# Kernel tuning notes

Measured on AMD Instinct MI355X. Metric: run time of the kernel, lower is better.

Reference implementation:

```python
import jax, jax.numpy as jnp
import numpy as np


def setup_inputs() -> dict:
    key = jax.random.key(0)
    k1, k2, k3 = jax.random.split(key, 3)
    C_in, C_out, K = 64, 64, 3
    x = jax.random.normal(k1, (32, C_in, 128, 128), dtype=jnp.float32)
    # Conv2d default init scale: U(-b, b) with b = 1/sqrt(fan_in)
    bound = 1.0 / np.sqrt(C_in * K * K)
    conv_weight = jax.random.uniform(k2, (C_out, C_in, K, K), dtype=jnp.float32,
                                     minval=-bound, maxval=bound)
    conv_bias = jax.random.uniform(k3, (C_out,), dtype=jnp.float32,
                                   minval=-bound, maxval=bound)
    return {"x": x, "conv_weight": conv_weight, "conv_bias": conv_bias}


def reference(x, conv_weight, conv_bias):
    # Conv2d, stride=1, padding=0 (VALID), NCHW/OIHW
    y = jax.lax.conv_general_dilated(
        x, conv_weight,
        window_strides=(1, 1), padding="VALID",
        dimension_numbers=("NCHW", "OIHW", "NCHW"),
    ) + conv_bias[None, :, None, None]
    # min over output channels (keepdim) then double tanh
    m = jnp.min(y, axis=1, keepdims=True)  # (N, 1, OH, OW)
    return jnp.tanh(jnp.tanh(m))
```

## Files before the change

kernel.cpp:

```cpp
#include <hip/hip_runtime.h>
#include <hip/hip_bf16.h>
#include <math.h>

typedef __attribute__((ext_vector_type(8))) short     short8;
typedef __attribute__((ext_vector_type(8))) __bf16    bf16x8;
typedef __attribute__((ext_vector_type(4))) float     f32x4;
typedef __attribute__((ext_vector_type(2))) unsigned int u32x2;

#define NB 32
#define CI 64
#define CO 64
#define H  128
#define W  128
#define OH 126
#define OW 126
#define HW (H*W)

#define TROWS 6
#define TCOLS 66
#define LDS_BYTES (TROWS*TCOLS*CI*2)

__device__ __forceinline__ unsigned int f2bf(float f) {
    unsigned int u = __builtin_bit_cast(unsigned int, f);
    u += 0x7fffu + ((u >> 16) & 1u);
    return u >> 16;
}

__device__ __forceinline__ unsigned int cvt_pk_bf16(float lo, float hi) {
    unsigned int r;
    asm("v_cvt_pk_bf16_f32 %0, %1, %2" : "=v"(r) : "v"(lo), "v"(hi));
    return r;
}

__device__ __forceinline__ float fast_tanh(float x) {
    float e = __builtin_amdgcn_exp2f(x * 2.8853900817779268f);
    float r = __builtin_amdgcn_rcpf(e + 1.0f);
    return 1.0f - 2.0f * r;
}

__global__ void wxform(const float* __restrict__ w, unsigned short* __restrict__ ws) {
    int tid = blockIdx.x * 256 + threadIdx.x;
    if (tid >= 18*4*64*8) return;
    int j   = tid & 7;
    int l   = (tid >> 3) & 63;
    int cf  = (tid >> 9) & 3;
    int ks  = tid >> 11;
    int co  = cf*16 + (l & 15);
    int ci  = (ks & 1)*32 + ((l >> 4) << 3) + j;
    int khw = ks >> 1;
    int kh  = khw / 3, kw = khw % 3;
    float v = w[co*(CI*9) + ci*9 + kh*3 + kw];
    ws[tid] = (unsigned short)f2bf(v);
}

__global__ __launch_bounds__(256, 3)
void conv_min_tanh(const float* __restrict__ x,
                   const unsigned short* __restrict__ wfrag,
                   const float* __restrict__ bias,
                   float* __restrict__ out) {
    __shared__ __align__(16) char xs[LDS_BYTES];

    const int lane   = threadIdx.x & 63;
    const int wv     = threadIdx.x >> 6;
    const int c0     = blockIdx.x * 64;
    const int r0     = blockIdx.y * 4;
    const int b      = blockIdx.z;

    const float* xb = x + b*CI*HW;

    float v[24][4];
    #pragma unroll
    for (int i = 0; i < 24; ++i) {
        const int task = wv + 4*i;
        const int r    = task >> 4;
        const int ci0  = (task & 15) << 2;
        const int gr   = r0 + r;
        v[i][0] = 0.f; v[i][1] = 0.f; v[i][2] = 0.f; v[i][3] = 0.f;
        if (gr < H) {
            const float* xp = xb + ci0*HW + gr*W + c0 + lane;
            v[i][0] = xp[0]; v[i][1] = xp[HW]; v[i][2] = xp[2*HW]; v[i][3] = xp[3*HW];
        }
    }
    const int t = threadIdx.x;
    float h0=0.f, h1=0.f, h2=0.f, h3=0.f;
    int hpix = 0, hci0 = 0;
    const bool hdo = t < 192;
    if (hdo) {
        const int r   = t >> 5;
        const int sub = t & 31;
        const int gc  = c0 + 64 + (sub & 1);
        hci0 = (sub >> 1) << 2;
        const int gr  = r0 + r;
        hpix = r*TCOLS + 64 + (sub & 1);
        if (gr < H && gc < W) {
            const float* xq = xb + hci0*HW + gr*W + gc;
            h0 = xq[0]; h1 = xq[HW]; h2 = xq[2*HW]; h3 = xq[3*HW];
        }
    }

    #pragma unroll
    for (int i = 0; i < 24; ++i) {
        const int task = wv + 4*i;
        const int r    = task >> 4;
        const int ci0  = (task & 15) << 2;
        int pix  = r*TCOLS + lane;
        int addr = (pix << 7) + (ci0 << 1);
        addr ^= (pix & 7) << 4;
        u32x2 pk; pk.x = cvt_pk_bf16(v[i][0], v[i][1]); pk.y = cvt_pk_bf16(v[i][2], v[i][3]);
        *(u32x2*)(xs + addr) = pk;
    }
    if (hdo) {
        int addr = (hpix << 7) + (hci0 << 1);
        addr ^= (hpix & 7) << 4;
        u32x2 qk; qk.x = cvt_pk_bf16(h0, h1); qk.y = cvt_pk_bf16(h2, h3);
        *(u32x2*)(xs + addr) = qk;
    }

    const short8* wp = (const short8*)wfrag;
    short8 wf[2][2][4];
    #pragma unroll
    for (int k2 = 0; k2 < 2; ++k2)
        #pragma unroll
        for (int cf = 0; cf < 4; ++cf)
            wf[0][k2][cf] = wp[(k2*4 + cf)*64 + lane];

    __syncthreads();

    const int orow = r0 + wv;
    if (orow >= OH) return;

    const int lane_c = lane & 15;
    const int hi16   = (lane >> 4) << 4;

    int abase[9][2];
    #pragma unroll
    for (int kh = 0; kh < 3; ++kh)
        #pragma unroll
        for (int kw = 0; kw < 3; ++kw) {
            const int pix  = (wv + kh)*TCOLS + lane_c + kw;
            const int swz  = (pix & 7) << 4;
            #pragma unroll
            for (int cih = 0; cih < 2; ++cih)
                abase[kh*3 + kw][cih] = (((pix << 7) + (cih << 6) + hi16)) ^ swz;
        }

    f32x4 acc[4][4];
    #pragma unroll
    for (int m = 0; m < 4; ++m)
        #pragma unroll
        for (int cf = 0; cf < 4; ++cf)
            acc[m][cf] = (f32x4){0.f, 0.f, 0.f, 0.f};

    #pragma unroll
    for (int ck = 0; ck < 9; ++ck) {
        const int buf = ck & 1;
        if (ck < 8) {
            #pragma unroll
            for (int k2 = 0; k2 < 2; ++k2)
                #pragma unroll
                for (int cf = 0; cf < 4; ++cf)
                    wf[buf ^ 1][k2][cf] = wp[(((ck + 1)*2 + k2)*4 + cf)*64 + lane];
        }
        #pragma unroll
        for (int k2 = 0; k2 < 2; ++k2) {
            #pragma unroll
            for (int m = 0; m < 4; ++m) {
                const short8 av = *(const short8*)(xs + abase[ck][k2] + m*2048);
                const bf16x8 a = __builtin_bit_cast(bf16x8, av);
                #pragma unroll
                for (int cf = 0; cf < 4; ++cf)
                    acc[m][cf] = __builtin_amdgcn_mfma_f32_16x16x32_bf16(
                        a, __builtin_bit_cast(bf16x8, wf[buf][k2][cf]), acc[m][cf], 0, 0, 0);
            }
        }
    }

    const float bs0 = bias[lane_c], bs1 = bias[16 + lane_c],
                bs2 = bias[32 + lane_c], bs3 = bias[48 + lane_c];
    float* outp = out + (b*OH + orow)*OW;
    #pragma unroll
    for (int m = 0; m < 4; ++m) {
        #pragma unroll
        for (int rg = 0; rg < 4; ++rg) {
            float v0 = fminf(fminf(acc[m][0][rg] + bs0, acc[m][1][rg] + bs1),
                             fminf(acc[m][2][rg] + bs2, acc[m][3][rg] + bs3));
            v0 = fminf(v0, __shfl_xor(v0, 1));
            v0 = fminf(v0, __shfl_xor(v0, 2));
            v0 = fminf(v0, __shfl_xor(v0, 4));
            v0 = fminf(v0, __shfl_xor(v0, 8));
            const float vt = fast_tanh(fast_tanh(v0));
            const int ocol = c0 + m*16 + ((lane >> 4) << 2) + rg;
            if (lane_c == 0 && ocol < OW) outp[ocol] = vt;
        }
    }
}

extern "C" void kernel_launch(void* const* d_in, const int* in_sizes, int n_in,
                              void* d_out, int out_size, void* d_ws, size_t ws_size,
                              hipStream_t stream) {
    const float* x    = (const float*)d_in[0];
    const float* w    = (const float*)d_in[1];
    const float* bias = (const float*)d_in[2];
    float* out        = (float*)d_out;
    unsigned short* wbuf = (unsigned short*)d_ws;

    wxform<<<dim3(144), dim3(256), 0, stream>>>(w, wbuf);
    conv_min_tanh<<<dim3(2, 32, NB), dim3(256), 0, stream>>>(x, wbuf, bias, out);
}
```

Before: 69.49 us.

## Split input-channel staging into two halves with padded LDS rows

The kernel now stages the input tile into LDS in two 32-channel halves, each followed by the MFMA work for that half, instead of loading all 64 channels up front. The LDS row stride is padded to 80 bytes in place of the XOR swizzle, which roughly halves the shared memory footprint, and launch bounds are raised to 4 blocks per CU. The goal is higher occupancy and lower register pressure, since the 96 staged floats per thread go away. The cost is an extra barrier, a serialized load-compute sequence within each block, and a weight prefetch that restarts for each half.

```diff
diff --git a/kernel.cpp b/kernel.cpp
--- a/kernel.cpp
+++ b/kernel.cpp
@@ -1,24 +1,22 @@
 #include <hip/hip_runtime.h>
 #include <hip/hip_bf16.h>
-#include <math.h>
 
-typedef __attribute__((ext_vector_type(8))) short     short8;
-typedef __attribute__((ext_vector_type(8))) __bf16    bf16x8;
-typedef __attribute__((ext_vector_type(4))) float     f32x4;
+typedef __attribute__((ext_vector_type(8))) short        short8;
+typedef __attribute__((ext_vector_type(8))) __bf16       bf16x8;
+typedef __attribute__((ext_vector_type(4))) float        f32x4;
 typedef __attribute__((ext_vector_type(2))) unsigned int u32x2;
 
 #define NB 32
 #define CI 64
-#define CO 64
 #define H  128
 #define W  128
 #define OH 126
 #define OW 126
 #define HW (H*W)
 
-#define TROWS 6
 #define TCOLS 66
-#define LDS_BYTES (TROWS*TCOLS*CI*2)
+#define RSTRIDE 80
+#define LDS_BYTES (6*TCOLS*RSTRIDE)
 
 __device__ __forceinline__ unsigned int f2bf(float f) {
     unsigned int u = __builtin_bit_cast(unsigned int, f);
@@ -26,7 +24,7 @@
     return u >> 16;
 }
 
-__device__ __forceinline__ unsigned int cvt_pk_bf16(float lo, float hi) {
+__device__ __forceinline__ unsigned int cvt_pk(float lo, float hi) {
     unsigned int r;
     asm("v_cvt_pk_bf16_f32 %0, %1, %2" : "=v"(r) : "v"(lo), "v"(hi));
     return r;
@@ -53,96 +51,26 @@
     ws[tid] = (unsigned short)f2bf(v);
 }
 
-__global__ __launch_bounds__(256, 3)
+__global__ __launch_bounds__(256, 4)
 void conv_min_tanh(const float* __restrict__ x,
                    const unsigned short* __restrict__ wfrag,
                    const float* __restrict__ bias,
                    float* __restrict__ out) {
     __shared__ __align__(16) char xs[LDS_BYTES];
 
-    const int lane   = threadIdx.x & 63;
-    const int wv     = threadIdx.x >> 6;
-    const int c0     = blockIdx.x * 64;
-    const int r0     = blockIdx.y * 4;
-    const int b      = blockIdx.z;
+    const int lane = threadIdx.x & 63;
+    const int wv   = threadIdx.x >> 6;
+    const int c0   = blockIdx.x * 64;
+    const int r0   = blockIdx.y * 4;
+    const int b    = blockIdx.z;
+    const float* xb = x + (size_t)b * CI * HW;
 
-    const float* xb = x + b*CI*HW;
-
-    float v[24][4];
-    #pragma unroll
-    for (int i = 0; i < 24; ++i) {
-        const int task = wv + 4*i;
-        const int r    = task >> 4;
-        const int ci0  = (task & 15) << 2;
-        const int gr   = r0 + r;
-        v[i][0] = 0.f; v[i][1] = 0.f; v[i][2] = 0.f; v[i][3] = 0.f;
-        if (gr < H) {
-            const float* xp = xb + ci0*HW + gr*W + c0 + lane;
-            v[i][0] = xp[0]; v[i][1] = xp[HW]; v[i][2] = xp[2*HW]; v[i][3] = xp[3*HW];
-        }
-    }
-    const int t = threadIdx.x;
-    float h0=0.f, h1=0.f, h2=0.f, h3=0.f;
-    int hpix = 0, hci0 = 0;
-    const bool hdo = t < 192;
-    if (hdo) {
-        const int r   = t >> 5;
-        const int sub = t & 31;
-        const int gc  = c0 + 64 + (sub & 1);
-        hci0 = (sub >> 1) << 2;
-        const int gr  = r0 + r;
-        hpix = r*TCOLS + 64 + (sub & 1);
-        if (gr < H && gc < W) {
-            const float* xq = xb + hci0*HW + gr*W + gc;
-            h0 = xq[0]; h1 = xq[HW]; h2 = xq[2*HW]; h3 = xq[3*HW];
-        }
-    }
-
-    #pragma unroll
-    for (int i = 0; i < 24; ++i) {
-        const int task = wv + 4*i;
-        const int r    = task >> 4;
-        const int ci0  = (task & 15) << 2;
-        int pix  = r*TCOLS + lane;
-        int addr = (pix << 7) + (ci0 << 1);
-        addr ^= (pix & 7) << 4;
-        u32x2 pk; pk.x = cvt_pk_bf16(v[i][0], v[i][1]); pk.y = cvt_pk_bf16(v[i][2], v[i][3]);
-        *(u32x2*)(xs + addr) = pk;
-    }
-    if (hdo) {
-        int addr = (hpix << 7) + (hci0 << 1);
-        addr ^= (hpix & 7) << 4;
-        u32x2 qk; qk.x = cvt_pk_bf16(h0, h1); qk.y = cvt_pk_bf16(h2, h3);
-        *(u32x2*)(xs + addr) = qk;
-    }
+    const int lane_c = lane & 15;
+    const int hi     = lane >> 4;
 
     const short8* wp = (const short8*)wfrag;
-    short8 wf[2][2][4];
-    #pragma unroll
-    for (int k2 = 0; k2 < 2; ++k2)
-        #pragma unroll
-        for (int cf = 0; cf < 4; ++cf)
-            wf[0][k2][cf] = wp[(k2*4 + cf)*64 + lane];
-
-    __syncthreads();
-
     const int orow = r0 + wv;
-    if (orow >= OH) return;
-
-    const int lane_c = lane & 15;
-    const int hi16   = (lane >> 4) << 4;
-
-    int abase[9][2];
-    #pragma unroll
-    for (int kh = 0; kh < 3; ++kh)
-        #pragma unroll
-        for (int kw = 0; kw < 3; ++kw) {
-            const int pix  = (wv + kh)*TCOLS + lane_c + kw;
-            const int swz  = (pix & 7) << 4;
-            #pragma unroll
-            for (int cih = 0; cih < 2; ++cih)
-                abase[kh*3 + kw][cih] = (((pix << 7) + (cih << 6) + hi16)) ^ swz;
-        }
+    const bool live = (orow < OH);
 
     f32x4 acc[4][4];
     #pragma unroll
@@ -151,29 +79,74 @@
         for (int cf = 0; cf < 4; ++cf)
             acc[m][cf] = (f32x4){0.f, 0.f, 0.f, 0.f};
 
+    int abase[9];
     #pragma unroll
-    for (int ck = 0; ck < 9; ++ck) {
-        const int buf = ck & 1;
-        if (ck < 8) {
+    for (int kh = 0; kh < 3; ++kh)
+        #pragma unroll
+        for (int kw = 0; kw < 3; ++kw)
+            abase[kh*3 + kw] = ((wv + kh)*TCOLS + lane_c + kw)*RSTRIDE + hi*16;
+
+    #pragma unroll
+    for (int cih = 0; cih < 2; ++cih) {
+        #pragma unroll
+        for (int i = 0; i < 12; ++i) {
+            const int tsk = wv + 4*i;
+            const int r   = tsk >> 3;
+            const int q   = tsk & 7;
+            const int gr  = r0 + r;
+            float v0=0.f, v1=0.f, v2=0.f, v3=0.f;
+            if (gr < H) {
+                const float* xp = xb + (size_t)(cih*32 + q*4)*HW + gr*W + c0 + lane;
+                v0 = xp[0]; v1 = xp[HW]; v2 = xp[2*HW]; v3 = xp[3*HW];
+            }
+            u32x2 pk; pk.x = cvt_pk(v0, v1); pk.y = cvt_pk(v2, v3);
+            *(u32x2*)(xs + (r*TCOLS + lane)*RSTRIDE + q*8) = pk;
+        }
+        if (threadIdx.x < 96) {
+            const int r   = threadIdx.x >> 4;
+            const int sub = threadIdx.x & 15;
+            const int cc  = sub & 1;
+            const int q   = sub >> 1;
+            const int gr  = r0 + r;
+            const int gc  = c0 + 64 + cc;
+            float v0=0.f, v1=0.f, v2=0.f, v3=0.f;
+            if (gr < H && gc < W) {
+                const float* xq = xb + (size_t)(cih*32 + q*4)*HW + gr*W + gc;
+                v0 = xq[0]; v1 = xq[HW]; v2 = xq[2*HW]; v3 = xq[3*HW];
+            }
+            u32x2 pk; pk.x = cvt_pk(v0, v1); pk.y = cvt_pk(v2, v3);
+            *(u32x2*)(xs + (r*TCOLS + 64 + cc)*RSTRIDE + q*8) = pk;
+        }
+        __syncthreads();
+
+        if (live) {
+            short8 wfb[2][4];
             #pragma unroll
-            for (int k2 = 0; k2 < 2; ++k2)
+            for (int cf = 0; cf < 4; ++cf)
+                wfb[0][cf] = wp[(cih*4 + cf)*64 + lane];
+            #pragma unroll
+            for (int khw = 0; khw < 9; ++khw) {
+                const int buf = khw & 1;
+                if (khw < 8) {
+                    #pragma unroll
+                    for (int cf = 0; cf < 4; ++cf)
+                        wfb[buf^1][cf] = wp[(((khw+1)*2 + cih)*4 + cf)*64 + lane];
+                }
                 #pragma unroll
-                for (int cf = 0; cf < 4; ++cf)
-                    wf[buf ^ 1][k2][cf] = wp[(((ck + 1)*2 + k2)*4 + cf)*64 + lane];
-        }
-        #pragma unroll
-        for (int k2 = 0; k2 < 2; ++k2) {
-            #pragma unroll
-            for (int m = 0; m < 4; ++m) {
-                const short8 av = *(const short8*)(xs + abase[ck][k2] + m*2048);
-                const bf16x8 a = __builtin_bit_cast(bf16x8, av);
-                #pragma unroll
-                for (int cf = 0; cf < 4; ++cf)
-                    acc[m][cf] = __builtin_amdgcn_mfma_f32_16x16x32_bf16(
-                        a, __builtin_bit_cast(bf16x8, wf[buf][k2][cf]), acc[m][cf], 0, 0, 0);
+                for (int m = 0; m < 4; ++m) {
+                    const short8 av = *(const short8*)(xs + abase[khw] + m*(16*RSTRIDE));
+                    const bf16x8 a = __builtin_bit_cast(bf16x8, av);
+                    #pragma unroll
+                    for (int cf = 0; cf < 4; ++cf)
+                        acc[m][cf] = __builtin_amdgcn_mfma_f32_16x16x32_bf16(
+                            a, __builtin_bit_cast(bf16x8, wfb[buf][cf]), acc[m][cf], 0, 0, 0);
+                }
             }
         }
+        if (cih == 0) __syncthreads();
     }
+
+    if (!live) return;
 
     const float bs0 = bias[lane_c], bs1 = bias[16 + lane_c],
                 bs2 = bias[32 + lane_c], bs3 = bias[48 + lane_c];
@@ -189,7 +162,7 @@
             v0 = fminf(v0, __shfl_xor(v0, 4));
             v0 = fminf(v0, __shfl_xor(v0, 8));
             const float vt = fast_tanh(fast_tanh(v0));
-            const int ocol = c0 + m*16 + ((lane >> 4) << 2) + rg;
+            const int ocol = c0 + m*16 + hi*4 + rg;
             if (lane_c == 0 && ocol < OW) outp[ocol] = vt;
         }
     }
```

New measurement: 76.78 us. 1.1x slower.
